# Performance work log

Measured on AMD Instinct MI355X. Metric: run time of the kernel, lower is better.

Reference implementation:

```python
import jax, jax.numpy as jnp
import numpy as np

B, V, L = 256, 128000, 2048
EPS = 1e-05


def setup_inputs() -> dict:
    key = jax.random.key(0)
    k1, k2, k3, k4, k5 = jax.random.split(key, 5)
    logits_next = jax.random.normal(k1, (B, V), jnp.float32)
    token_ids = jax.random.randint(k2, (B, L), 0, V, jnp.int32)
    presence_penalties = jax.random.uniform(k3, (B,), jnp.float32) * 1.5
    temperatures = jax.random.uniform(k4, (B,), jnp.float32, 0.5, 1.5)
    # make first quarter of the batch greedy (temperature == 0)
    temperatures = temperatures.at[: B // 4].set(0.0)
    u = jax.random.uniform(k5, (B, V), jnp.float32, 1e-9, 1.0)
    gumbel = -jnp.log(-jnp.log(u))  # Gumbel(0,1) noise for multinomial sampling
    return {
        "logits_next": logits_next,
        "token_ids": token_ids,
        "presence_penalties": presence_penalties,
        "temperatures": temperatures,
        "gumbel": gumbel,
    }


def reference(logits_next, token_ids, presence_penalties, temperatures, gumbel):
    Bn, Vn = logits_next.shape
    # presence mask: 1.0 where token id appeared in the history (counts > 0)
    rows = jnp.arange(Bn, dtype=jnp.int32)[:, None]  # [B,1]
    presence = jnp.zeros((Bn, Vn), logits_next.dtype).at[rows, token_ids].set(1.0)
    penalized = logits_next - presence_penalties[:, None] * presence

    greedy = temperatures < EPS  # [B]
    safe_t = jnp.where(greedy, jnp.float32(1.0), temperatures)
    scaled = penalized / safe_t[:, None]

    # greedy rows: plain argmax; sample rows: Gumbel-max == multinomial(softmax)
    greedy_tok = jnp.argmax(penalized, axis=-1)
    sampled_tok = jnp.argmax(scaled + gumbel, axis=-1)
    token_ids_next = jnp.where(greedy, greedy_tok, sampled_tok)
    return token_ids_next.astype(jnp.int32)
```

## Files before the change

kernel.cpp:

```cpp
#include <hip/hip_runtime.h>
#include <math.h>

#define BATCH 256
#define VOCAB 128000
#define HIST  2048
#define EPS_T 1e-5f

#define SEGS 25
#define SEG_ELEMS (VOCAB / SEGS)
#define SEG_VEC   (SEG_ELEMS / 4)
#define SEG_WORDS (SEG_ELEMS / 32)
#define BBLOCK 256
#define BWAVES (BBLOCK / 64)

__device__ __forceinline__ unsigned fkey(float f) {
    unsigned b = __float_as_uint(f);
    return (b & 0x80000000u) ? ~b : (b | 0x80000000u);
}

__device__ __forceinline__ void upd(float s, int idx, float& best, int& besti) {
    if (s > best || (s == best && idx < besti)) { best = s; besti = idx; }
}

__device__ __forceinline__ void body4(float4 l, unsigned w, int sh, float pen,
                                      int idx0, float& best, int& besti) {
    float e[4] = {l.x, l.y, l.z, l.w};
    #pragma unroll
    for (int j = 0; j < 4; j++) {
        float present = (float)((w >> (sh + j)) & 1u);
        float p = e[j] - pen * present;
        upd(p, idx0 + j, best, besti);
    }
}

__device__ __forceinline__ void body4s(float4 l, float4 g, unsigned w, int sh,
                                       float pen, float temp,
                                       int idx0, float& best, int& besti) {
    float e[4]  = {l.x, l.y, l.z, l.w};
    float gv[4] = {g.x, g.y, g.z, g.w};
    #pragma unroll
    for (int j = 0; j < 4; j++) {
        float present = (float)((w >> (sh + j)) & 1u);
        float p = e[j] - pen * present;
        float s = p / temp + gv[j];
        upd(s, idx0 + j, best, besti);
    }
}

__device__ __forceinline__ void setbit(int t, int segBase, unsigned* smask) {
    unsigned u = (unsigned)(t - segBase);
    if (u < (unsigned)SEG_ELEMS)
        atomicOr(&smask[u >> 5], 1u << (u & 31));
}

__global__ __launch_bounds__(BBLOCK, 1) void fused_scan(
    const float* __restrict__ logits,
    const float* __restrict__ gumbel,
    const int*   __restrict__ token_ids,
    const float* __restrict__ penalties,
    const float* __restrict__ temps,
    unsigned long long* __restrict__ keys)
{
    __shared__ unsigned smask[SEG_WORDS];
    __shared__ float wval[BWAVES];
    __shared__ int   widx[BWAVES];

    const int blk = blockIdx.x;
    const int b   = blk / SEGS;
    const int seg = blk - b * SEGS;
    const int tid = threadIdx.x;

    const float pen    = penalties[b];
    const float temp   = temps[b];
    const bool  greedy = (temp < EPS_T);

    const int segBase = seg * SEG_ELEMS;

    if (tid < SEG_WORDS) smask[tid] = 0u;

    const int4* rt = (const int4*)(token_ids + (size_t)b * HIST);
    int4 ta = rt[tid];
    int4 tb = rt[tid + BBLOCK];
    __builtin_amdgcn_sched_barrier(0);

    const float4* lg = (const float4*)(logits + (size_t)b * VOCAB) + seg * SEG_VEC;
    const float4* gm = (const float4*)(gumbel + (size_t)b * VOCAB) + seg * SEG_VEC;

    float best  = -INFINITY;
    int   besti = 0x7fffffff;
    const int sh    = (tid * 4) & 31;
    const int abs0  = segBase + tid * 4;
    const int wbase = tid >> 3;

    if (greedy) {
        float4 l0 = lg[tid];
        float4 l1 = lg[tid + 1 * BBLOCK];
        float4 l2 = lg[tid + 2 * BBLOCK];
        float4 l3 = lg[tid + 3 * BBLOCK];
        float4 l4 = lg[tid + 4 * BBLOCK];
        __builtin_amdgcn_sched_barrier(0);

        __syncthreads();
        setbit(ta.x, segBase, smask); setbit(ta.y, segBase, smask);
        setbit(ta.z, segBase, smask); setbit(ta.w, segBase, smask);
        setbit(tb.x, segBase, smask); setbit(tb.y, segBase, smask);
        setbit(tb.z, segBase, smask); setbit(tb.w, segBase, smask);
        __syncthreads();

        unsigned w0 = smask[wbase];
        unsigned w1 = smask[wbase + 32];
        unsigned w2 = smask[wbase + 64];
        unsigned w3 = smask[wbase + 96];
        unsigned w4 = smask[wbase + 128];
        body4(l0, w0, sh, pen, abs0 + 0 * BBLOCK * 4, best, besti);
        body4(l1, w1, sh, pen, abs0 + 1 * BBLOCK * 4, best, besti);
        body4(l2, w2, sh, pen, abs0 + 2 * BBLOCK * 4, best, besti);
        body4(l3, w3, sh, pen, abs0 + 3 * BBLOCK * 4, best, besti);
        body4(l4, w4, sh, pen, abs0 + 4 * BBLOCK * 4, best, besti);
    } else {
        float4 l0 = lg[tid];
        float4 l1 = lg[tid + 1 * BBLOCK];
        float4 l2 = lg[tid + 2 * BBLOCK];
        float4 l3 = lg[tid + 3 * BBLOCK];
        float4 l4 = lg[tid + 4 * BBLOCK];
        float4 g0 = gm[tid];
        float4 g1 = gm[tid + 1 * BBLOCK];
        float4 g2 = gm[tid + 2 * BBLOCK];
        float4 g3 = gm[tid + 3 * BBLOCK];
        float4 g4 = gm[tid + 4 * BBLOCK];
        __builtin_amdgcn_sched_barrier(0);

        __syncthreads();
        setbit(ta.x, segBase, smask); setbit(ta.y, segBase, smask);
        setbit(ta.z, segBase, smask); setbit(ta.w, segBase, smask);
        setbit(tb.x, segBase, smask); setbit(tb.y, segBase, smask);
        setbit(tb.z, segBase, smask); setbit(tb.w, segBase, smask);
        __syncthreads();

        unsigned w0 = smask[wbase];
        unsigned w1 = smask[wbase + 32];
        unsigned w2 = smask[wbase + 64];
        unsigned w3 = smask[wbase + 96];
        unsigned w4 = smask[wbase + 128];
        body4s(l0, g0, w0, sh, pen, temp, abs0 + 0 * BBLOCK * 4, best, besti);
        body4s(l1, g1, w1, sh, pen, temp, abs0 + 1 * BBLOCK * 4, best, besti);
        body4s(l2, g2, w2, sh, pen, temp, abs0 + 2 * BBLOCK * 4, best, besti);
        body4s(l3, g3, w3, sh, pen, temp, abs0 + 3 * BBLOCK * 4, best, besti);
        body4s(l4, g4, w4, sh, pen, temp, abs0 + 4 * BBLOCK * 4, best, besti);
    }

    #pragma unroll
    for (int off = 32; off > 0; off >>= 1) {
        float ov = __shfl_down(best, off, 64);
        int   oi = __shfl_down(besti, off, 64);
        if (ov > best || (ov == best && oi < besti)) { best = ov; besti = oi; }
    }
    const int wave = tid >> 6, lane = tid & 63;
    if (lane == 0) { wval[wave] = best; widx[wave] = besti; }
    __syncthreads();

    if (tid == 0) {
        #pragma unroll
        for (int wv = 1; wv < BWAVES; wv++) {
            if (wval[wv] > best || (wval[wv] == best && widx[wv] < besti)) {
                best = wval[wv]; besti = widx[wv];
            }
        }
        unsigned long long key =
            ((unsigned long long)fkey(best) << 32) | (unsigned)(~besti);
        atomicMax(keys + b, key);
    }
}

__global__ void decode_kernel(const unsigned long long* __restrict__ keys,
                              int* __restrict__ out)
{
    const int b = threadIdx.x;
    out[b] = (int)(~(unsigned)keys[b]);
}

extern "C" void kernel_launch(void* const* d_in, const int* in_sizes, int n_in,
                              void* d_out, int out_size, void* d_ws, size_t ws_size,
                              hipStream_t stream) {
    const float* logits    = (const float*)d_in[0];
    const int*   token_ids = (const int*)d_in[1];
    const float* penalties = (const float*)d_in[2];
    const float* temps     = (const float*)d_in[3];
    const float* gumbel    = (const float*)d_in[4];
    int* out = (int*)d_out;

    unsigned long long* keys = (unsigned long long*)d_ws;

    hipMemsetAsync(keys, 0, BATCH * sizeof(unsigned long long), stream);

    fused_scan<<<BATCH * SEGS, BBLOCK, 0, stream>>>(logits, gumbel, token_ids,
                                                    penalties, temps, keys);
    decode_kernel<<<1, BATCH, 0, stream>>>(keys, out);
}
```

Baseline: 268.1 us.

## Use fewer, larger vocab segments per row with a software-prefetched streaming loop

```diff
diff --git a/kernel.cpp b/kernel.cpp
--- a/kernel.cpp
+++ b/kernel.cpp
@@ -6,12 +6,14 @@
 #define HIST  2048
 #define EPS_T 1e-5f
 
-#define SEGS 25
+#define SEGS 5
 #define SEG_ELEMS (VOCAB / SEGS)
 #define SEG_VEC   (SEG_ELEMS / 4)
 #define SEG_WORDS (SEG_ELEMS / 32)
 #define BBLOCK 256
 #define BWAVES (BBLOCK / 64)
+#define NCHUNK (SEG_ELEMS / (BBLOCK * 4))
+#define PF 4
 
 __device__ __forceinline__ unsigned fkey(float f) {
     unsigned b = __float_as_uint(f);
@@ -76,12 +78,19 @@
 
     const int segBase = seg * SEG_ELEMS;
 
-    if (tid < SEG_WORDS) smask[tid] = 0u;
-
     const int4* rt = (const int4*)(token_ids + (size_t)b * HIST);
     int4 ta = rt[tid];
     int4 tb = rt[tid + BBLOCK];
-    __builtin_amdgcn_sched_barrier(0);
+
+    #pragma unroll
+    for (int i = tid; i < SEG_WORDS; i += BBLOCK) smask[i] = 0u;
+    __syncthreads();
+
+    setbit(ta.x, segBase, smask); setbit(ta.y, segBase, smask);
+    setbit(ta.z, segBase, smask); setbit(ta.w, segBase, smask);
+    setbit(tb.x, segBase, smask); setbit(tb.y, segBase, smask);
+    setbit(tb.z, segBase, smask); setbit(tb.w, segBase, smask);
+    __syncthreads();
 
     const float4* lg = (const float4*)(logits + (size_t)b * VOCAB) + seg * SEG_VEC;
     const float4* gm = (const float4*)(gumbel + (size_t)b * VOCAB) + seg * SEG_VEC;
@@ -93,60 +102,34 @@
     const int wbase = tid >> 3;
 
     if (greedy) {
-        float4 l0 = lg[tid];
-        float4 l1 = lg[tid + 1 * BBLOCK];
-        float4 l2 = lg[tid + 2 * BBLOCK];
-        float4 l3 = lg[tid + 3 * BBLOCK];
-        float4 l4 = lg[tid + 4 * BBLOCK];
-        __builtin_amdgcn_sched_barrier(0);
-
-        __syncthreads();
-        setbit(ta.x, segBase, smask); setbit(ta.y, segBase, smask);
-        setbit(ta.z, segBase, smask); setbit(ta.w, segBase, smask);
-        setbit(tb.x, segBase, smask); setbit(tb.y, segBase, smask);
-        setbit(tb.z, segBase, smask); setbit(tb.w, segBase, smask);
-        __syncthreads();
-
-        unsigned w0 = smask[wbase];
-        unsigned w1 = smask[wbase + 32];
-        unsigned w2 = smask[wbase + 64];
-        unsigned w3 = smask[wbase + 96];
-        unsigned w4 = smask[wbase + 128];
-        body4(l0, w0, sh, pen, abs0 + 0 * BBLOCK * 4, best, besti);
-        body4(l1, w1, sh, pen, abs0 + 1 * BBLOCK * 4, best, besti);
-        body4(l2, w2, sh, pen, abs0 + 2 * BBLOCK * 4, best, besti);
-        body4(l3, w3, sh, pen, abs0 + 3 * BBLOCK * 4, best, besti);
-        body4(l4, w4, sh, pen, abs0 + 4 * BBLOCK * 4, best, besti);
+        float4 lb[NCHUNK];
+        #pragma unroll
+        for (int k = 0; k < PF; ++k) lb[k] = lg[tid + k * BBLOCK];
+        #pragma unroll
+        for (int k = 0; k < NCHUNK; ++k) {
+            if (k + PF < NCHUNK) lb[k + PF] = lg[tid + (k + PF) * BBLOCK];
+            __builtin_amdgcn_sched_barrier(0);
+            unsigned w = smask[wbase + 32 * k];
+            body4(lb[k], w, sh, pen, abs0 + k * BBLOCK * 4, best, besti);
+        }
     } else {
-        float4 l0 = lg[tid];
-        float4 l1 = lg[tid + 1 * BBLOCK];
-        float4 l2 = lg[tid + 2 * BBLOCK];
-        float4 l3 = lg[tid + 3 * BBLOCK];
-        float4 l4 = lg[tid + 4 * BBLOCK];
-        float4 g0 = gm[tid];
-        float4 g1 = gm[tid + 1 * BBLOCK];
-        float4 g2 = gm[tid + 2 * BBLOCK];
-        float4 g3 = gm[tid + 3 * BBLOCK];
-        float4 g4 = gm[tid + 4 * BBLOCK];
-        __builtin_amdgcn_sched_barrier(0);
-
-        __syncthreads();
-        setbit(ta.x, segBase, smask); setbit(ta.y, segBase, smask);
-        setbit(ta.z, segBase, smask); setbit(ta.w, segBase, smask);
-        setbit(tb.x, segBase, smask); setbit(tb.y, segBase, smask);
-        setbit(tb.z, segBase, smask); setbit(tb.w, segBase, smask);
-        __syncthreads();
-
-        unsigned w0 = smask[wbase];
-        unsigned w1 = smask[wbase + 32];
-        unsigned w2 = smask[wbase + 64];
-        unsigned w3 = smask[wbase + 96];
-        unsigned w4 = smask[wbase + 128];
-        body4s(l0, g0, w0, sh, pen, temp, abs0 + 0 * BBLOCK * 4, best, besti);
-        body4s(l1, g1, w1, sh, pen, temp, abs0 + 1 * BBLOCK * 4, best, besti);
-        body4s(l2, g2, w2, sh, pen, temp, abs0 + 2 * BBLOCK * 4, best, besti);
-        body4s(l3, g3, w3, sh, pen, temp, abs0 + 3 * BBLOCK * 4, best, besti);
-        body4s(l4, g4, w4, sh, pen, temp, abs0 + 4 * BBLOCK * 4, best, besti);
+        float4 lb[NCHUNK], gb[NCHUNK];
+        #pragma unroll
+        for (int k = 0; k < PF; ++k) {
+            lb[k] = lg[tid + k * BBLOCK];
+            gb[k] = gm[tid + k * BBLOCK];
+        }
+        #pragma unroll
+        for (int k = 0; k < NCHUNK; ++k) {
+            if (k + PF < NCHUNK) {
+                lb[k + PF] = lg[tid + (k + PF) * BBLOCK];
+                gb[k + PF] = gm[tid + (k + PF) * BBLOCK];
+            }
+            __builtin_amdgcn_sched_barrier(0);
+            unsigned w = smask[wbase + 32 * k];
+            body4s(lb[k], gb[k], w, sh, pen, temp,
+                   abs0 + k * BBLOCK * 4, best, besti);
+        }
     }
 
     #pragma unroll
```

Measured after the change: 276.3 us. +3.0%, slower.
